# Kernel optimization log

Hardware: AMD Instinct MI355X
Metric: run time of the kernel (lower is better)

Reference implementation:

```python
import jax, jax.numpy as jnp
import numpy as np

B, T_IN, T_OUT, N, FEAT = 32, 96, 96, 512, 8
HID = 512
GRID_SIZE, SPLINE_ORDER = 5, 3
GRID_RANGE = (-1.0, 1.0)


def _make_grid():
    # matches KANLinear.create_grid: identical row per in_feature, so keep 1-D
    h = (GRID_RANGE[1] - GRID_RANGE[0]) / GRID_SIZE
    return jnp.arange(-SPLINE_ORDER, GRID_SIZE + SPLINE_ORDER + 1, dtype=jnp.float32) * h + GRID_RANGE[0]


def _b_splines(x, grid):
    # x: [M, in_features]; de Boor-Cox recursion, order SPLINE_ORDER
    x = x[..., None]  # [M, in, 1]
    bases = ((x >= grid[:-1]) & (x < grid[1:])).astype(x.dtype)
    for k in range(1, SPLINE_ORDER + 1):
        left = (x - grid[:-(k + 1)]) / (grid[k:-1] - grid[:-(k + 1)])
        right = (grid[k + 1:] - x) / (grid[k + 1:] - grid[1:-k])
        bases = left * bases[..., :-1] + right * bases[..., 1:]
    return bases  # [M, in, grid_size + spline_order]


def setup_inputs() -> dict:
    key = jax.random.key(0)
    ks = jax.random.split(key, 12)
    s = 0.05
    return {
        "X": jax.random.normal(ks[0], (B, T_IN, N, FEAT), jnp.float32),
        "Y": jax.random.normal(ks[1], (B, T_OUT, N, FEAT), jnp.float32),
        "Wx": jax.random.normal(ks[2], (HID, T_IN * FEAT), jnp.float32) * s,
        "bx": jax.random.normal(ks[3], (HID,), jnp.float32) * s,
        "Wy": jax.random.normal(ks[4], (HID, T_OUT * FEAT), jnp.float32) * s,
        "by": jax.random.normal(ks[5], (HID,), jnp.float32) * s,
        "base_w": jax.random.normal(ks[6], (64, 2 * HID), jnp.float32) * s,
        "spline_w": jax.random.normal(ks[7], (64, 2 * HID, GRID_SIZE + SPLINE_ORDER), jnp.float32) * s,
        "spline_scaler": jax.random.normal(ks[8], (64, 2 * HID), jnp.float32) * s,
        "Wf": jax.random.normal(ks[9], (T_OUT * FEAT, 64), jnp.float32) * s,
        "bf": jax.random.normal(ks[10], (T_OUT * FEAT,), jnp.float32) * s,
    }


def reference(X, Y, Wx, bx, Wy, by, base_w, spline_w, spline_scaler, Wf, bf):
    # [B, T, N, F] -> [B, N, T*F]
    Xf = jnp.transpose(X, (0, 2, 1, 3)).reshape(B, N, T_IN * FEAT)
    Yf = jnp.transpose(Y, (0, 2, 1, 3)).reshape(B, N, T_OUT * FEAT)
    Hx = jnp.tanh(Xf @ Wx.T + bx)
    Hy = jnp.tanh(Yf @ Wy.T + by)
    h = jnp.concatenate([Hx, Hy], axis=-1).reshape(B * N, 2 * HID)

    grid = _make_grid()
    base_out = jax.nn.silu(h) @ base_w.T
    scaled_sw = spline_w * spline_scaler[..., None]  # [out, in, coeff]
    spline_out = jnp.einsum("mik,oik->mo", _b_splines(h, grid), scaled_sw)
    kan_out = (base_out + spline_out).reshape(B, N, 64)

    out = kan_out @ Wf.T + bf  # [B, N, T_OUT*FEAT]
    out = out.reshape(B, N, T_OUT, FEAT)
    return jnp.transpose(out, (0, 2, 1, 3))  # [B, T_OUT, N, FEAT]
```

## Files before the change

kernel.cpp:

```cpp
#include <hip/hip_runtime.h>
#include <cmath>

#define B_    32
#define T_    96
#define N_    512
#define F_    8
#define TF_   768
#define HID_  512
#define M_    16384
#define KIN_  1024
#define KS_   8

typedef short short8 __attribute__((ext_vector_type(8)));
typedef _Float16 halfx8 __attribute__((ext_vector_type(8)));
typedef float f32x4  __attribute__((ext_vector_type(4)));
typedef float f32x2  __attribute__((ext_vector_type(2)));
typedef unsigned int  uintx4 __attribute__((ext_vector_type(4)));
typedef unsigned long long ulongx2 __attribute__((ext_vector_type(2)));
typedef unsigned short      ushort_t;
typedef unsigned int        uint_t;
typedef unsigned long long  ulong_t;

#define HT_B     0ull
#define WQ_B     33554432ull
#define WB_B     34734080ull
#define SH_B     36306944ull
#define KANR_B   61472768ull
#define WFQ_B    63569920ull

__device__ __constant__ float KC[8] = {
    -0.2818252f, -0.2770046f, -0.2237417f, -0.1031025f,
     0.0968975f,  0.3762583f,  0.7229954f,  1.1181747f };

static __device__ inline uint_t  fbits(float f){ return __builtin_bit_cast(uint_t, f); }
static __device__ inline ushort_t f2b(float f){
    uint_t u = fbits(f);
    return (ushort_t)((u + 0x7fffu + ((u >> 16) & 1u)) >> 16);
}
static __device__ inline float b2f(ushort_t h){ return __builtin_bit_cast(float, (uint_t)h << 16); }
static __device__ inline ulong_t pack4(float4 v){
    return (ulong_t)f2b(v.x) | ((ulong_t)f2b(v.y) << 16) |
           ((ulong_t)f2b(v.z) << 32) | ((ulong_t)f2b(v.w) << 48);
}
static __device__ inline ulong_t pack4t(float4 v){
    uint_t d0 = (fbits(v.x) >> 16) | (fbits(v.y) & 0xffff0000u);
    uint_t d1 = (fbits(v.z) >> 16) | (fbits(v.w) & 0xffff0000u);
    return (ulong_t)d0 | ((ulong_t)d1 << 32);
}
static __device__ inline float fast_tanh(float x){
    const float e = __expf(2.0f * x);
    return 1.0f - 2.0f / (e + 1.0f);
}
static __device__ inline void gload_lds16(const void* g, void* l){
    __builtin_amdgcn_global_load_lds(
        (const __attribute__((address_space(1))) unsigned int*)g,
        (__attribute__((address_space(3))) unsigned int*)l, 16, 0, 0);
}

__global__ __launch_bounds__(256) void pack_wq(
    const float* __restrict__ base_w,
    const float* __restrict__ spline_w,
    const float* __restrict__ scaler,
    ushort_t* __restrict__ wq)
{
    const int e = blockIdx.x * 256 + threadIdx.x;
    const int j  = e & 7;
    const int ln = (e >> 3) & 63;
    const int ct = (e >> 9) & 3;
    const int t  = (e >> 11) & 3;
    const int ss = (e >> 13) & 7;
    const int ks = e >> 16;
    const int o = ct * 16 + (ln & 15);
    const int g = ln >> 4;
    const int i = ks * 128 + ss * 16 + t * 4 + g;
    const float v = spline_w[(o * KIN_ + i) * 8 + j] * scaler[o * KIN_ + i]
                  + base_w[o * KIN_ + i] * KC[j];
    wq[e] = f2b(v);
}

__global__ __launch_bounds__(256) void pack_wb2(
    const float* __restrict__ Wx,
    const float* __restrict__ Wy,
    ushort_t* __restrict__ wb)
{
    const int e = blockIdx.x * 256 + threadIdx.x;
    const float v = (e < 512 * TF_) ? Wx[e] : Wy[e - 512 * TF_];
    wb[e] = f2b(v);
}

__global__ __launch_bounds__(256) void pack_wfq(
    const float* __restrict__ Wf, ushort_t* __restrict__ wfq)
{
    const int e = blockIdx.x * 256 + threadIdx.x;
    const int jj  = e & 7;
    const int ln  = (e >> 3) & 63;
    const int rt  = (e >> 9) & 3;
    const int s   = (e >> 11) & 1;
    const int wvt = (e >> 12) & 1;
    const int tb  = e >> 13;
    const int tf = tb * 128 + wvt * 64 + rt * 16 + (ln & 15);
    const int o  = s * 32 + (ln >> 4) * 8 + jj;
    wfq[e] = f2b(Wf[(size_t)tf * 64 + o]);
}

__global__ __launch_bounds__(256) void xcvt_kernel(
    const float* __restrict__ Xs, ushort_t* __restrict__ xbf)
{
    __shared__ __align__(16) char lds[32 * 1552];
    const int tid = threadIdx.x;
    const int n0  = blockIdx.x * 32;
    const int bb  = blockIdx.y;
    const int nl  = (tid & 63) >> 1;
    const int f4  = (tid & 1) * 4;
    const int tq  = tid >> 6;
    #pragma unroll 4
    for (int u = 0; u < 24; u++) {
        const int t = u * 4 + tq;
        const float4 v = *(const float4*)(Xs + (size_t)bb * (T_ * N_ * F_)
                                             + (size_t)t * (N_ * F_)
                                             + (size_t)(n0 + nl) * F_ + f4);
        *(ulong_t*)(lds + nl * 1552 + t * 16 + f4 * 2) = pack4t(v);
    }
    __syncthreads();
    #pragma unroll 4
    for (int u = 0; u < 12; u++) {
        const int c   = u * 256 + tid;
        const int row = c / 96;
        const int col = c - row * 96;
        const uintx4 val = *(const uintx4*)(lds + row * 1552 + col * 16);
        *(uintx4*)(xbf + (size_t)(bb * 512 + n0 + row) * TF_ + col * 8) = val;
    }
}

__global__ __launch_bounds__(512, 2) void gemm_tanh_v7(
    const ushort_t* __restrict__ xbf,
    const ushort_t* __restrict__ wb,
    const float* __restrict__ bias,
    ushort_t* __restrict__ ht, int z)
{
    __shared__ __align__(16) char smem[32768];

    const int tid = threadIdx.x;
    const int wv  = tid >> 6;
    const int ln  = tid & 63;
    const int lr  = ln & 15;
    const int hi  = ln >> 4;
    const int wm  = wv >> 2;
    const int wj  = wv & 3;

    const int m0  = blockIdx.x * 128;
    const int jl0 = blockIdx.y * 128;
    const int j0  = z * 512 + jl0;

    const int r_l = ln >> 3;
    const int ck  = ((ln & 7) ^ r_l) * 8;

    f32x4 acc[4][2] = {};

    for (int kt = 0; kt < 12; kt++) {
        __syncthreads();
        #pragma unroll
        for (int s = 0; s < 2; s++) {
            const int reg = s * 8 + wv;
            const int row = reg * 8 + r_l;
            gload_lds16(xbf + (size_t)(m0 + row) * TF_ + kt * 64 + ck,
                        smem + reg * 1024 + ln * 16);
            gload_lds16(wb + (size_t)(j0 + row) * TF_ + kt * 64 + ck,
                        smem + 16384 + reg * 1024 + ln * 16);
        }
        __syncthreads();

        #pragma unroll
        for (int h = 0; h < 2; h++) {
            const int g = h * 4 + hi;
            short8 a[4], b[2];
            #pragma unroll
            for (int rt = 0; rt < 4; rt++) {
                const int r = wm * 64 + rt * 16 + lr;
                a[rt] = *(short8*)(smem + r * 128 + ((g ^ (r & 7)) * 16));
            }
            #pragma unroll
            for (int ct = 0; ct < 2; ct++) {
                const int r = wj * 32 + ct * 16 + lr;
                b[ct] = *(short8*)(smem + 16384 + r * 128 + ((g ^ (r & 7)) * 16));
            }
            #pragma unroll
            for (int rt = 0; rt < 4; rt++)
                #pragma unroll
                for (int ct = 0; ct < 2; ct++)
                    acc[rt][ct] = __builtin_amdgcn_mfma_f32_16x16x32_bf16(
                        a[rt], b[ct], acc[rt][ct], 0, 0, 0);
        }
    }

    __syncthreads();
    #pragma unroll
    for (int ct = 0; ct < 2; ct++) {
        const int j = wj * 32 + ct * 16 + lr;
        const float bvv = bias[jl0 + j];
        #pragma unroll
        for (int rt = 0; rt < 4; rt++) {
            const f32x4 v = acc[rt][ct];
            float4 tv;
            tv.x = fast_tanh(v[0] + bvv);
            tv.y = fast_tanh(v[1] + bvv);
            tv.z = fast_tanh(v[2] + bvv);
            tv.w = fast_tanh(v[3] + bvv);
            const int slot = wm * 8 + rt * 2 + (hi >> 1);
            *(ulong_t*)(smem + j * 256 + ((slot ^ (j & 15)) * 16) + (hi & 1) * 8)
                = pack4(tv);
        }
    }
    __syncthreads();
    {
        const int j  = tid >> 2;
        const int q4 = tid & 3;
        ushort_t* dst = ht + (size_t)(j0 + j) * M_ + m0 + q4 * 32;
        #pragma unroll
        for (int w = 0; w < 4; w++) {
            const int slot = q4 * 4 + w;
            short8 val = *(short8*)(smem + j * 256 + ((slot ^ (j & 15)) * 16));
            *(short8*)(dst + w * 8) = val;
        }
    }
}

static __device__ inline short8 shift_pack(float b0, float b1, float b2, float b3, int si)
{
    const uint_t d0 = (fbits(b0) >> 16) | (fbits(b1) & 0xffff0000u);
    const uint_t d1 = (fbits(b2) >> 16) | (fbits(b3) & 0xffff0000u);
    const ulong_t P = (ulong_t)d0 | ((ulong_t)d1 << 32);
    const int sh = si << 4;
    const ulong_t Plo = P << (sh & 63);
    const ulong_t Phi = P >> ((64 - sh) & 63);
    ulongx2 pr;
    pr.x = (si == 4) ? 0ull : Plo;
    pr.y = (si == 0) ? 0ull : ((si == 4) ? P : Phi);
    return __builtin_bit_cast(short8, pr);
}

static __device__ inline void eval_bases2(float x0, float x1, short8& a0, short8& a1)
{
    f32x2 x = {x0, x1};
    f32x2 v = x * 2.5f + 2.5f;
    f32x2 sf = __builtin_elementwise_floor(v);
    sf = __builtin_elementwise_min(sf, (f32x2){4.0f, 4.0f});
    const f32x2 u  = v - sf;
    const f32x2 u2 = u * u;
    const f32x2 u3 = u2 * u;
    const f32x2 omu = 1.0f - u;
    const f32x2 omu3 = omu * omu * omu;
    const f32x2 B0 = omu3 * (1.0f / 6.0f);
    const f32x2 B3 = u3 * (1.0f / 6.0f);
    const f32x2 B1 = (u3 * 0.5f + (2.0f / 3.0f)) - u2;
    const f32x2 B2 = 1.0f - B0 - B1 - B3;
    a0 = shift_pack(B0[0], B1[0], B2[0], B3[0], (int)sf[0]);
    a1 = shift_pack(B0[1], B1[1], B2[1], B3[1], (int)sf[1]);
}

__global__ __launch_bounds__(256) void kan_v10b(
    const ushort_t* __restrict__ ht,
    const ushort_t* __restrict__ wq,
    _Float16* __restrict__ kanp)
{
    __shared__ __align__(16) char lds[49152];

    const int tid = threadIdx.x;
    const int wv  = tid >> 6;
    const int ln  = tid & 63;
    const int g   = ln >> 4;
    const int lr  = ln & 15;
    const int m0  = blockIdx.x * 128;
    const int ks  = blockIdx.y;
    const int iB  = ks * 128;

    const ushort_t* wqk = wq + (size_t)ks * 65536;

    #pragma unroll
    for (int c = 0; c < 8; c++) {
        const int ll = wv * 8 + c;
        const int il = ll * 4 + (ln >> 4);
        const int chunk = ln & 15;
        const int rowst = (chunk ^ ((il & 3) << 1)) * 8;
        gload_lds16(ht + (size_t)(iB + il) * M_ + m0 + rowst,
                    lds + ll * 1024 + (ln & 15) * 16 + (ln >> 4) * 256);
    }
    gload_lds16(wqk + (size_t)wv * 512 + ln * 8,
                lds + 32768 + wv * 1024 + ln * 16);
    gload_lds16(wqk + (size_t)(4 + wv) * 512 + ln * 8,
                lds + 32768 + (4 + wv) * 1024 + ln * 16);
    short8 wA0 = *(const short8*)(wqk + (size_t)(8 + wv) * 512 + ln * 8);
    short8 wA1 = *(const short8*)(wqk + (size_t)(12 + wv) * 512 + ln * 8);
    short8 wB0 = *(const short8*)(wqk + (size_t)(16 + wv) * 512 + ln * 8);
    short8 wB1 = *(const short8*)(wqk + (size_t)(20 + wv) * 512 + ln * 8);
    __syncthreads();

    const int hb0 = g * 256 + ((wv * 64 + lr * 2) ^ (g << 5));
    const int hb1 = g * 256 + ((wv * 64 + 32 + lr * 2) ^ (g << 5));

    f32x4 acc[2][4] = {};

    #pragma unroll 4
    for (int p = 0; p < 16; ++p) {
        char* rb = lds + 32768 + (p & 1) * 8192;
        short8 bfr[8];
        #pragma unroll
        for (int f = 0; f < 8; f++)
            bfr[f] = *(short8*)(rb + f * 1024 + ln * 16);

        if (p < 15) {
            char* wbuf = lds + 32768 + ((p + 1) & 1) * 8192;
            *(short8*)(wbuf + wv * 1024 + ln * 16)       = wA0;
            *(short8*)(wbuf + (4 + wv) * 1024 + ln * 16) = wA1;
        }
        wA0 = wB0; wA1 = wB1;
        if (p < 13) {
            wB0 = *(const short8*)(wqk + (size_t)((p + 3) * 8 + wv) * 512 + ln * 8);
            wB1 = *(const short8*)(wqk + (size_t)((p + 3) * 8 + 4 + wv) * 512 + ln * 8);
        }

        const int itA = 2 * p, itB = 2 * p + 1;
        short8 a0, a1, a2, a3;
        eval_bases2(b2f(*(const ushort_t*)(lds + hb0 + itA * 1024)),
                    b2f(*(const ushort_t*)(lds + hb1 + itA * 1024)), a0, a1);
        eval_bases2(b2f(*(const ushort_t*)(lds + hb0 + itB * 1024)),
                    b2f(*(const ushort_t*)(lds + hb1 + itB * 1024)), a2, a3);

        acc[0][0] = __builtin_amdgcn_mfma_f32_16x16x32_bf16(a0, bfr[0], acc[0][0], 0, 0, 0);
        acc[0][1] = __builtin_amdgcn_mfma_f32_16x16x32_bf16(a0, bfr[1], acc[0][1], 0, 0, 0);
        acc[0][2] = __builtin_amdgcn_mfma_f32_16x16x32_bf16(a0, bfr[2], acc[0][2], 0, 0, 0);
        acc[0][3] = __builtin_amdgcn_mfma_f32_16x16x32_bf16(a0, bfr[3], acc[0][3], 0, 0, 0);
        acc[1][0] = __builtin_amdgcn_mfma_f32_16x16x32_bf16(a1, bfr[0], acc[1][0], 0, 0, 0);
        acc[1][1] = __builtin_amdgcn_mfma_f32_16x16x32_bf16(a1, bfr[1], acc[1][1], 0, 0, 0);
        acc[1][2] = __builtin_amdgcn_mfma_f32_16x16x32_bf16(a1, bfr[2], acc[1][2], 0, 0, 0);
        acc[1][3] = __builtin_amdgcn_mfma_f32_16x16x32_bf16(a1, bfr[3], acc[1][3], 0, 0, 0);
        acc[0][0] = __builtin_amdgcn_mfma_f32_16x16x32_bf16(a2, bfr[4], acc[0][0], 0, 0, 0);
        acc[0][1] = __builtin_amdgcn_mfma_f32_16x16x32_bf16(a2, bfr[5], acc[0][1], 0, 0, 0);
        acc[0][2] = __builtin_amdgcn_mfma_f32_16x16x32_bf16(a2, bfr[6], acc[0][2], 0, 0, 0);
        acc[0][3] = __builtin_amdgcn_mfma_f32_16x16x32_bf16(a2, bfr[7], acc[0][3], 0, 0, 0);
        acc[1][0] = __builtin_amdgcn_mfma_f32_16x16x32_bf16(a3, bfr[4], acc[1][0], 0, 0, 0);
        acc[1][1] = __builtin_amdgcn_mfma_f32_16x16x32_bf16(a3, bfr[5], acc[1][1], 0, 0, 0);
        acc[1][2] = __builtin_amdgcn_mfma_f32_16x16x32_bf16(a3, bfr[6], acc[1][2], 0, 0, 0);
        acc[1][3] = __builtin_amdgcn_mfma_f32_16x16x32_bf16(a3, bfr[7], acc[1][3], 0, 0, 0);

        __syncthreads();
    }

    #pragma unroll
    for (int rt = 0; rt < 2; rt++) {
        #pragma unroll
        for (int ct = 0; ct < 4; ct++) {
            const int o = ct * 16 + lr;
            #pragma unroll
            for (int q = 0; q < 4; q++) {
                const size_t row = (size_t)(m0 + wv * 32 + rt * 16 + g * 4 + q);
                kanp[(size_t)ks * (M_ * 64) + row * 64 + o] = (_Float16)acc[rt][ct][q];
            }
        }
    }
}

__global__ __launch_bounds__(256) void reduce_kan(
    const _Float16* __restrict__ kanp, ushort_t* __restrict__ kanr)
{
    const int e8 = blockIdx.x * 256 + threadIdx.x;
    const size_t base = (size_t)e8 * 8;
    float s[8] = {};
    #pragma unroll
    for (int p = 0; p < KS_; p++) {
        const halfx8 v = *(const halfx8*)(kanp + (size_t)p * (M_ * 64) + base);
        #pragma unroll
        for (int j = 0; j < 8; j++) s[j] += (float)v[j];
    }
    float4 s0 = make_float4(s[0], s[1], s[2], s[3]);
    float4 s1 = make_float4(s[4], s[5], s[6], s[7]);
    ulongx2 outv;
    outv.x = pack4(s0);
    outv.y = pack4(s1);
    *(ulongx2*)(kanr + base) = outv;
}

__global__ __launch_bounds__(256) void final_v2(
    const ushort_t* __restrict__ kanr,
    const ushort_t* __restrict__ wfq,
    const float* __restrict__ bf,
    float* __restrict__ out)
{
    const int tid = threadIdx.x;
    const int wv  = tid >> 6;
    const int ln  = tid & 63;
    const int lr  = ln & 15;
    const int hi  = ln >> 4;
    const int wvm = wv >> 1;
    const int wvt = wv & 1;
    const int mb  = blockIdx.x;
    const int tb  = blockIdx.y;

    f32x4 acc[4][4] = {};

    #pragma unroll
    for (int s = 0; s < 2; s++) {
        short8 afr[4], bfr[4];
        #pragma unroll
        for (int rt = 0; rt < 4; rt++) {
            const size_t idx = ((size_t)(((tb * 2 + wvt) * 2 + s) * 4 + rt)) * 64 + ln;
            afr[rt] = ((const short8*)wfq)[idx];
        }
        #pragma unroll
        for (int ct = 0; ct < 4; ct++) {
            const int m = mb * 128 + wvm * 64 + ct * 16 + lr;
            bfr[ct] = *(const short8*)(kanr + (size_t)m * 64 + s * 32 + hi * 8);
        }
        #pragma unroll
        for (int rt = 0; rt < 4; rt++)
            #pragma unroll
            for (int ct = 0; ct < 4; ct++)
                acc[rt][ct] = __builtin_amdgcn_mfma_f32_16x16x32_bf16(
                    afr[rt], bfr[ct], acc[rt][ct], 0, 0, 0);
    }

    #pragma unroll
    for (int rt = 0; rt < 4; rt++) {
        const int tf0 = tb * 128 + wvt * 64 + rt * 16 + hi * 4;
        const float4 b4 = *(const float4*)&bf[tf0];
        const int t  = tf0 >> 3;
        const int f0 = tf0 & 7;
        #pragma unroll
        for (int ct = 0; ct < 4; ct++) {
            const int m = mb * 128 + wvm * 64 + ct * 16 + lr;
            const int bb = m >> 9;
            const int n  = m & 511;
            const f32x4 v = acc[rt][ct];
            float4 o4 = make_float4(v[0] + b4.x, v[1] + b4.y, v[2] + b4.z, v[3] + b4.w);
            *(float4*)&out[(size_t)bb * (T_ * N_ * F_)
                           + (size_t)t * (N_ * F_)
                           + (size_t)n * F_ + f0] = o4;
        }
    }
}

extern "C" void kernel_launch(void* const* d_in, const int* in_sizes, int n_in,
                              void* d_out, int out_size, void* d_ws, size_t ws_size,
                              hipStream_t stream)
{
    const float* X      = (const float*)d_in[0];
    const float* Y      = (const float*)d_in[1];
    const float* Wx     = (const float*)d_in[2];
    const float* bx     = (const float*)d_in[3];
    const float* Wy     = (const float*)d_in[4];
    const float* by     = (const float*)d_in[5];
    const float* base_w = (const float*)d_in[6];
    const float* spline_w = (const float*)d_in[7];
    const float* spline_scaler = (const float*)d_in[8];
    const float* Wf     = (const float*)d_in[9];
    const float* bf     = (const float*)d_in[10];

    float* out = (float*)d_out;
    ushort_t* ht   = (ushort_t*)((char*)d_ws + HT_B);
    ushort_t* wq   = (ushort_t*)((char*)d_ws + WQ_B);
    ushort_t* wb   = (ushort_t*)((char*)d_ws + WB_B);
    ushort_t* xbf  = (ushort_t*)((char*)d_ws + SH_B);
    _Float16* kanp = (_Float16*)((char*)d_ws + SH_B);
    ushort_t* kanr = (ushort_t*)((char*)d_ws + KANR_B);
    ushort_t* wfq  = (ushort_t*)((char*)d_ws + WFQ_B);

    pack_wq<<<2048, 256, 0, stream>>>(base_w, spline_w, spline_scaler, wq);
    pack_wb2<<<3072, 256, 0, stream>>>(Wx, Wy, wb);
    pack_wfq<<<192, 256, 0, stream>>>(Wf, wfq);

    xcvt_kernel<<<dim3(16, 32), 256, 0, stream>>>(X, xbf);
    gemm_tanh_v7<<<dim3(128, 4), 512, 0, stream>>>(xbf, wb, bx, ht, 0);
    xcvt_kernel<<<dim3(16, 32), 256, 0, stream>>>(Y, xbf);
    gemm_tanh_v7<<<dim3(128, 4), 512, 0, stream>>>(xbf, wb, by, ht, 1);

    kan_v10b<<<dim3(M_ / 128, KS_), 256, 0, stream>>>(ht, wq, kanp);
    reduce_kan<<<512, 256, 0, stream>>>(kanp, kanr);
    final_v2<<<dim3(128, 6), 256, 0, stream>>>(kanr, wfq, bf, out);
}
```

Measured before the change: 127.6 us.

## Fuse fp32-to-bf16 transpose into hidden GEMM and merge X/Y launches

The separate xcvt transpose/convert kernels are removed, and the GEMM now loads fp32 X/Y directly from global memory, packs it to bf16 and writes it into the swizzled LDS tile. The next k-tile's A values are register-prefetched while the current tile is computed. The two per-input GEMM launches become a single 1024-block launch, with an XCD-aware block-index remap that selects X or Y and the matching bias. This drops the bf16 intermediate round trip and two launches, at the cost of extra registers and strided fp32 loads inside the GEMM.

```diff
diff --git a/kernel.cpp b/kernel.cpp
--- a/kernel.cpp
+++ b/kernel.cpp
@@ -103,42 +103,24 @@
     wfq[e] = f2b(Wf[(size_t)tf * 64 + o]);
 }
 
-__global__ __launch_bounds__(256) void xcvt_kernel(
-    const float* __restrict__ Xs, ushort_t* __restrict__ xbf)
-{
-    __shared__ __align__(16) char lds[32 * 1552];
-    const int tid = threadIdx.x;
-    const int n0  = blockIdx.x * 32;
-    const int bb  = blockIdx.y;
-    const int nl  = (tid & 63) >> 1;
-    const int f4  = (tid & 1) * 4;
-    const int tq  = tid >> 6;
-    #pragma unroll 4
-    for (int u = 0; u < 24; u++) {
-        const int t = u * 4 + tq;
-        const float4 v = *(const float4*)(Xs + (size_t)bb * (T_ * N_ * F_)
-                                             + (size_t)t * (N_ * F_)
-                                             + (size_t)(n0 + nl) * F_ + f4);
-        *(ulong_t*)(lds + nl * 1552 + t * 16 + f4 * 2) = pack4t(v);
-    }
-    __syncthreads();
-    #pragma unroll 4
-    for (int u = 0; u < 12; u++) {
-        const int c   = u * 256 + tid;
-        const int row = c / 96;
-        const int col = c - row * 96;
-        const uintx4 val = *(const uintx4*)(lds + row * 1552 + col * 16);
-        *(uintx4*)(xbf + (size_t)(bb * 512 + n0 + row) * TF_ + col * 8) = val;
-    }
-}
-
-__global__ __launch_bounds__(512, 2) void gemm_tanh_v7(
-    const ushort_t* __restrict__ xbf,
+__global__ __launch_bounds__(512, 2) void gemm_tanh_v10(
+    const float* __restrict__ X, const float* __restrict__ Y,
     const ushort_t* __restrict__ wb,
-    const float* __restrict__ bias,
-    ushort_t* __restrict__ ht, int z)
+    const float* __restrict__ bx, const float* __restrict__ by,
+    ushort_t* __restrict__ ht)
 {
     __shared__ __align__(16) char smem[32768];
+
+    const int bid = blockIdx.x;
+    const int xcd = bid & 7;
+    const int q   = bid >> 3;
+    const int jb  = q & 3;
+    const int pi  = xcd * 32 + (q >> 2);
+    const int z   = pi >> 7;
+    const int mb  = pi & 127;
+
+    const float* Xs   = z ? Y : X;
+    const float* bias = z ? by : bx;
 
     const int tid = threadIdx.x;
     const int wv  = tid >> 6;
@@ -148,27 +130,57 @@
     const int wm  = wv >> 2;
     const int wj  = wv & 3;
 
-    const int m0  = blockIdx.x * 128;
-    const int jl0 = blockIdx.y * 128;
+    const int jl0 = jb * 128;
+    const int m0  = mb * 128;
     const int j0  = z * 512 + jl0;
+    const int bb  = m0 >> 9;
+    const int n0  = m0 & 511;
+
+    const int arow = tid >> 2;
+    const int aq   = tid & 3;
+    const float* abase = Xs + (size_t)bb * (T_ * N_ * F_)
+                            + (size_t)(n0 + arow) * F_;
 
     const int r_l = ln >> 3;
     const int ck  = ((ln & 7) ^ r_l) * 8;
 
     f32x4 acc[4][2] = {};
 
+    float4 pv0, pv1, pv2, pv3;
+    {
+        const size_t t0 = (size_t)(aq * 2) * (N_ * F_);
+        pv0 = *(const float4*)(abase + t0);
+        pv1 = *(const float4*)(abase + t0 + 4);
+        pv2 = *(const float4*)(abase + t0 + (N_ * F_));
+        pv3 = *(const float4*)(abase + t0 + (N_ * F_) + 4);
+    }
+
     for (int kt = 0; kt < 12; kt++) {
         __syncthreads();
+        {
+            ulongx2 w0, w1;
+            w0.x = pack4t(pv0); w0.y = pack4t(pv1);
+            w1.x = pack4t(pv2); w1.y = pack4t(pv3);
+            const int s0 = aq * 2;
+            *(ulongx2*)(smem + arow * 128 + ((s0       ^ (arow & 7)) * 16)) = w0;
+            *(ulongx2*)(smem + arow * 128 + (((s0 + 1) ^ (arow & 7)) * 16)) = w1;
+        }
         #pragma unroll
         for (int s = 0; s < 2; s++) {
             const int reg = s * 8 + wv;
             const int row = reg * 8 + r_l;
-            gload_lds16(xbf + (size_t)(m0 + row) * TF_ + kt * 64 + ck,
-                        smem + reg * 1024 + ln * 16);
             gload_lds16(wb + (size_t)(j0 + row) * TF_ + kt * 64 + ck,
                         smem + 16384 + reg * 1024 + ln * 16);
         }
         __syncthreads();
+
+        if (kt < 11) {
+            const size_t t0 = (size_t)((kt + 1) * 8 + aq * 2) * (N_ * F_);
+            pv0 = *(const float4*)(abase + t0);
+            pv1 = *(const float4*)(abase + t0 + 4);
+            pv2 = *(const float4*)(abase + t0 + (N_ * F_));
+            pv3 = *(const float4*)(abase + t0 + (N_ * F_) + 4);
+        }
 
         #pragma unroll
         for (int h = 0; h < 2; h++) {
@@ -459,7 +471,6 @@
     ushort_t* ht   = (ushort_t*)((char*)d_ws + HT_B);
     ushort_t* wq   = (ushort_t*)((char*)d_ws + WQ_B);
     ushort_t* wb   = (ushort_t*)((char*)d_ws + WB_B);
-    ushort_t* xbf  = (ushort_t*)((char*)d_ws + SH_B);
     _Float16* kanp = (_Float16*)((char*)d_ws + SH_B);
     ushort_t* kanr = (ushort_t*)((char*)d_ws + KANR_B);
     ushort_t* wfq  = (ushort_t*)((char*)d_ws + WFQ_B);
@@ -468,10 +479,7 @@
     pack_wb2<<<3072, 256, 0, stream>>>(Wx, Wy, wb);
     pack_wfq<<<192, 256, 0, stream>>>(Wf, wfq);
 
-    xcvt_kernel<<<dim3(16, 32), 256, 0, stream>>>(X, xbf);
-    gemm_tanh_v7<<<dim3(128, 4), 512, 0, stream>>>(xbf, wb, bx, ht, 0);
-    xcvt_kernel<<<dim3(16, 32), 256, 0, stream>>>(Y, xbf);
-    gemm_tanh_v7<<<dim3(128, 4), 512, 0, stream>>>(xbf, wb, by, ht, 1);
+    gemm_tanh_v10<<<1024, 512, 0, stream>>>(X, Y, wb, bx, by, ht);
 
     kan_v10b<<<dim3(M_ / 128, KS_), 256, 0, stream>>>(ht, wq, kanp);
     reduce_kan<<<512, 256, 0, stream>>>(kanp, kanr);
```

Result: slower. 131.3 us (+2.9%).
